# Performance work log

Measured on AMD Instinct MI355X. Metric: run time of the kernel, lower is better.

The kernel has to match this reference:

```python
import jax, jax.numpy as jnp
import numpy as np

NUM_EMBEDDINGS = 8192
EMBEDDING_DIM = 256
COMMITMENT_COST = 0.25
DECAY = 0.99
EPSILON = 1e-05


def setup_inputs() -> dict:
    key = jax.random.key(0)
    k1, k2 = jax.random.split(key)
    inputs = jax.random.normal(k1, (16384, EMBEDDING_DIM), dtype=jnp.float32)
    embedding = jax.random.normal(k2, (NUM_EMBEDDINGS, EMBEDDING_DIM), dtype=jnp.float32)
    ema_cluster_size = jnp.zeros((NUM_EMBEDDINGS,), dtype=jnp.float32)
    ema_w = embedding  # buffer initialized as a clone of the codebook
    return {"inputs": inputs, "embedding": embedding,
            "ema_cluster_size": ema_cluster_size, "ema_w": ema_w}


def reference(inputs, embedding, ema_cluster_size, ema_w):
    N, D = inputs.shape
    K = embedding.shape[0]

    x2 = jnp.sum(inputs * inputs, axis=1, keepdims=True)          # [N,1]
    e2 = jnp.sum(embedding * embedding, axis=1)                   # [K]
    d2 = x2 + e2[None, :] - 2.0 * (inputs @ embedding.T)          # [N,K]
    idx = jnp.argmin(d2, axis=1)                                  # [N]

    quantized_raw = embedding[idx]                                # [N,D]
    encodings = jax.nn.one_hot(idx, K, dtype=jnp.float32)         # [N,K]

    # cluster statistics (scatter-add instead of dense one-hot matmul)
    counts = jax.ops.segment_sum(jnp.ones((N,), jnp.float32), idx, num_segments=K)  # [K]
    dw = jax.ops.segment_sum(inputs, idx, num_segments=K)                            # [K,D]

    # EMA codebook update (training branch)
    ecs = ema_cluster_size * DECAY + (1.0 - DECAY) * counts
    n = jnp.sum(ecs)
    ecs = (ecs + EPSILON) / (n + K * EPSILON) * n
    new_ema_w = ema_w * DECAY + (1.0 - DECAY) * dw
    new_embedding = new_ema_w / ecs[:, None]

    # commitment loss (quantized detached)
    e_latent_loss = jnp.mean((jax.lax.stop_gradient(quantized_raw) - inputs) ** 2)
    loss = COMMITMENT_COST * e_latent_loss

    # straight-through estimator
    quantized = inputs + jax.lax.stop_gradient(quantized_raw - inputs)

    avg_probs = counts / N
    perplexity = jnp.exp(-jnp.sum(avg_probs * jnp.log(avg_probs + 1e-10)))

    return (loss, quantized, perplexity, encodings, new_embedding, ecs, new_ema_w)
```

## Files before the change

kernel.cpp:

```cpp
#include <hip/hip_runtime.h>
#include <cstdint>
#include <cstddef>

#define NROWS 16384
#define DDIM  256
#define KCODES 8192
#define MARGIN 1.5f

typedef short bf16x8 __attribute__((ext_vector_type(8)));
typedef float f32x4 __attribute__((ext_vector_type(4)));
typedef float f32x2 __attribute__((ext_vector_type(2)));

__device__ inline unsigned short f2bf(float f) {
  unsigned int u = __float_as_uint(f);
  return (unsigned short)((u + 0x7fffu + ((u >> 16) & 1u)) >> 16);
}

__device__ inline void ins2(float v, int i, float& v1, int& i1, float& v2, int& i2) {
  bool b1 = (v < v1) || (v == v1 && i < i1);
  bool b2 = (v < v2) || (v == v2 && i < i2);
  if (b1) { v2 = v1; i2 = i1; v1 = v; i1 = i; }
  else if (b2) { v2 = v; i2 = i; }
}

__global__ void k_prep(const float* __restrict__ inp, const float* __restrict__ emb,
                       unsigned short* __restrict__ Xb, unsigned short* __restrict__ Ebt,
                       float* __restrict__ x2, float* __restrict__ e2) {
  int wave = threadIdx.x >> 6, lane = threadIdx.x & 63;
  int row = blockIdx.x * 4 + wave;
  bool isx = row < NROWS;
  const float* src = isx ? (inp + (size_t)row * DDIM) : (emb + (size_t)(row - NROWS) * DDIM);
  float4 v = ((const float4*)src)[lane];
  ushort4 u; u.x = f2bf(v.x); u.y = f2bf(v.y); u.z = f2bf(v.z); u.w = f2bf(v.w);
  if (isx) {
    *(ushort4*)&Xb[(size_t)row * DDIM + lane * 4] = u;
  } else {
    int c = row - NROWS, ct = c >> 4, lc = c & 15;
    size_t off = (size_t)ct * 4096 + (lane >> 3) * 512 + lc * 32 + (lane & 7) * 4;
    *(ushort4*)&Ebt[off] = u;
  }
  float s = v.x * v.x + v.y * v.y + v.z * v.z + v.w * v.w;
#pragma unroll
  for (int o = 32; o >= 1; o >>= 1) s += __shfl_down(s, o, 64);
  if (lane == 0) { if (isx) x2[row] = s; else e2[row - NROWS] = s; }
}

#define DECL_SLOT(s) \
  float v1_##s = 3.4e38f, v2_##s = 3.4e38f; \
  int i1_##s = 0x7fffffff, i2_##s = 0x7fffffff;

#define UPD(s, a) { \
  float d = fmaf(-2.0f, (a), e2c); \
  if (d < v1_##s) { v2_##s = v1_##s; i2_##s = i1_##s; v1_##s = d; i1_##s = col; } \
  else if (d < v2_##s) { v2_##s = d; i2_##s = col; } }

#define RED_SLOT(s, mi, r) { \
  float a1 = v1_##s, a2 = v2_##s; int b1 = i1_##s, b2 = i2_##s; \
  for (int off = 1; off < 16; off <<= 1) { \
    float o1 = __shfl_xor(a1, off, 64); int p1 = __shfl_xor(b1, off, 64); \
    float o2 = __shfl_xor(a2, off, 64); int p2 = __shfl_xor(b2, off, 64); \
    ins2(o1, p1, a1, b1, a2, b2); ins2(o2, p2, a1, b1, a2, b2); } \
  if (lcol == 0) { \
    int row = row0 + (mi) * 16 + quad * 4 + (r); \
    size_t o = ((size_t)row * 8 + slice) * 2; \
    candv[o] = a1; candv[o + 1] = a2; candi[o] = b1; candi[o + 1] = b2; } }

__global__ __launch_bounds__(256, 2) void k_dist(
    const unsigned short* __restrict__ Xb, const unsigned short* __restrict__ Ebt,
    const float* __restrict__ e2,
    float* __restrict__ candv, int* __restrict__ candi) {
  const int lane = threadIdx.x & 63;
  const int w = threadIdx.x >> 6;
  const int lcol = lane & 15, quad = lane >> 4;
  const int row0 = (blockIdx.x >> 3) * 128 + w * 32;
  const int slice = blockIdx.x & 7;

  const unsigned short* ApA = Xb + (size_t)(row0 + lcol) * DDIM + quad * 8;
  const unsigned short* ApB = ApA + 16 * DDIM;
#define DECL_A(q) \
  bf16x8 A0_##q = *(const bf16x8*)(ApA + (q) * 32); \
  bf16x8 A1_##q = *(const bf16x8*)(ApB + (q) * 32);
  DECL_A(0) DECL_A(1) DECL_A(2) DECL_A(3) DECL_A(4) DECL_A(5) DECL_A(6) DECL_A(7)

  DECL_SLOT(0) DECL_SLOT(1) DECL_SLOT(2) DECL_SLOT(3)
  DECL_SLOT(4) DECL_SLOT(5) DECL_SLOT(6) DECL_SLOT(7)

  const unsigned short* Bbase = Ebt + (size_t)slice * 64 * 4096 + lcol * 32 + quad * 8;
  const float* e2p = e2 + slice * 1024 + lcol;
  const int colbase = slice * 1024 + lcol;

#pragma unroll 2
  for (int t = 0; t < 64; ++t) {
    const unsigned short* Bt = Bbase + (size_t)t * 4096;
    bf16x8 B0 = *(const bf16x8*)(Bt);
    bf16x8 B1 = *(const bf16x8*)(Bt + 512);
    bf16x8 B2 = *(const bf16x8*)(Bt + 1024);
    bf16x8 B3 = *(const bf16x8*)(Bt + 1536);
    bf16x8 B4 = *(const bf16x8*)(Bt + 2048);
    bf16x8 B5 = *(const bf16x8*)(Bt + 2560);
    bf16x8 B6 = *(const bf16x8*)(Bt + 3072);
    bf16x8 B7 = *(const bf16x8*)(Bt + 3584);
    float e2c = e2p[t * 16];
    f32x4 acc0 = {0.f, 0.f, 0.f, 0.f};
    f32x4 acc1 = {0.f, 0.f, 0.f, 0.f};
#define MM(q) \
    acc0 = __builtin_amdgcn_mfma_f32_16x16x32_bf16(A0_##q, B##q, acc0, 0, 0, 0); \
    acc1 = __builtin_amdgcn_mfma_f32_16x16x32_bf16(A1_##q, B##q, acc1, 0, 0, 0);
    MM(0) MM(1) MM(2) MM(3) MM(4) MM(5) MM(6) MM(7)
#undef MM
    const int col = colbase + t * 16;
    UPD(0, acc0[0]) UPD(1, acc0[1]) UPD(2, acc0[2]) UPD(3, acc0[3])
    UPD(4, acc1[0]) UPD(5, acc1[1]) UPD(6, acc1[2]) UPD(7, acc1[3])
  }

  RED_SLOT(0, 0, 0) RED_SLOT(1, 0, 1) RED_SLOT(2, 0, 2) RED_SLOT(3, 0, 3)
  RED_SLOT(4, 1, 0) RED_SLOT(5, 1, 1) RED_SLOT(6, 1, 2) RED_SLOT(7, 1, 3)
}

__global__ void k_selscat(const float* __restrict__ inp, const float* __restrict__ emb,
                          const float* __restrict__ x2, const float* __restrict__ e2,
                          const float* __restrict__ candv, const int* __restrict__ candi,
                          int* __restrict__ idxb,
                          float* __restrict__ out_quant,
                          float* __restrict__ counts, float* __restrict__ dw,
                          float* __restrict__ loss_acc) {
  __shared__ float wsum[4];
  int w = threadIdx.x >> 6, lane = threadIdx.x & 63;
  int row = blockIdx.x * 4 + w;
  float cv = 3.4e38f;
  int ci = 0x7fffffff;
  if (lane < 16) { cv = candv[(size_t)row * 16 + lane]; ci = candi[(size_t)row * 16 + lane]; }
  float m = cv;
#pragma unroll
  for (int o = 32; o >= 1; o >>= 1) m = fminf(m, __shfl_xor(m, o, 64));
  float thr = m + MARGIN;
  unsigned long long b = __ballot(cv <= thr);
  float4 x = *(const float4*)(inp + (size_t)row * DDIM + lane * 4);
  float x2r = x2[row];
  float bestv = 3.4e38f;
  int besti = 0x7fffffff;
  while (b) {
    int src = __ffsll(b) - 1; b &= b - 1;
    int j = __shfl(ci, src, 64);
    float4 e4 = *(const float4*)(emb + (size_t)j * DDIM + lane * 4);
    float p = x.x * e4.x + x.y * e4.y + x.z * e4.z + x.w * e4.w;
#pragma unroll
    for (int o = 32; o >= 1; o >>= 1) p += __shfl_xor(p, o, 64);
    float d2 = (x2r + e2[j]) - 2.0f * p;
    if (d2 < bestv || (d2 == bestv && j < besti)) { bestv = d2; besti = j; }
  }
  const int j = besti;
  if (lane == 0) idxb[row] = j;

  float4 e = *(const float4*)(emb + (size_t)j * DDIM + lane * 4);
  size_t qo = (size_t)row * DDIM + lane * 4;
  __builtin_nontemporal_store(x.x + (e.x - x.x), out_quant + qo + 0);
  __builtin_nontemporal_store(x.y + (e.y - x.y), out_quant + qo + 1);
  __builtin_nontemporal_store(x.z + (e.z - x.z), out_quant + qo + 2);
  __builtin_nontemporal_store(x.w + (e.w - x.w), out_quant + qo + 3);
  size_t dwo = (size_t)j * DDIM + lane * 4;
  atomicAdd(&dw[dwo + 0], x.x);
  atomicAdd(&dw[dwo + 1], x.y);
  atomicAdd(&dw[dwo + 2], x.z);
  atomicAdd(&dw[dwo + 3], x.w);
  float d0 = e.x - x.x, d1 = e.y - x.y, d2 = e.z - x.z, d3 = e.w - x.w;
  float s = d0 * d0 + d1 * d1 + d2 * d2 + d3 * d3;
#pragma unroll
  for (int o = 32; o >= 1; o >>= 1) s += __shfl_down(s, o, 64);
  if (lane == 0) {
    atomicAdd(&counts[j], 1.0f);
    wsum[w] = s;
  }
  __syncthreads();
  if (threadIdx.x == 0) atomicAdd(loss_acc, wsum[0] + wsum[1] + wsum[2] + wsum[3]);
}

__global__ __launch_bounds__(256) void k_enc(const int* __restrict__ idxb,
                                             float* __restrict__ out_enc) {
  const int row = blockIdx.x;
  const int tid = threadIdx.x;
  const int j = idxb[row];
  float* base = out_enc + (size_t)row * KCODES;
#pragma unroll
  for (int i = 0; i < 8; ++i) {
    int q = i * 256 + tid;
    if (q < 2047) {
      int f0 = 2 + q * 4;
      f32x4 v;
      v[0] = (j == f0 + 0) ? 1.0f : 0.0f;
      v[1] = (j == f0 + 1) ? 1.0f : 0.0f;
      v[2] = (j == f0 + 2) ? 1.0f : 0.0f;
      v[3] = (j == f0 + 3) ? 1.0f : 0.0f;
      __builtin_nontemporal_store(v, (f32x4*)(base + f0));
    }
  }
  if (tid == 0) {
    f32x2 head = {j == 0 ? 1.0f : 0.0f, j == 1 ? 1.0f : 0.0f};
    f32x2 tail = {j == 8190 ? 1.0f : 0.0f, j == 8191 ? 1.0f : 0.0f};
    __builtin_nontemporal_store(head, (f32x2*)base);
    __builtin_nontemporal_store(tail, (f32x2*)(base + 8190));
  }
}

__global__ void k_stats(const float* __restrict__ counts, const float* __restrict__ ema_cs,
                        const float* __restrict__ loss_acc,
                        float* __restrict__ out_loss, float* __restrict__ out_perp,
                        float* __restrict__ out_ecs) {
  __shared__ float red[8];
  int tid = threadIdx.x;
  float ln = 0.0f, lp = 0.0f;
  for (int k = tid; k < KCODES; k += 256) {
    float c = counts[k];
    float er = ema_cs[k] * 0.99f + 0.01f * c;
    ln += er;
    float p = c * (1.0f / 16384.0f);
    lp += p * logf(p + 1e-10f);
  }
  int lane = tid & 63, wave = tid >> 6;
#pragma unroll
  for (int o = 32; o >= 1; o >>= 1) {
    ln += __shfl_down(ln, o, 64);
    lp += __shfl_down(lp, o, 64);
  }
  if (lane == 0) { red[wave] = ln; red[wave + 4] = lp; }
  __syncthreads();
  float n = red[0] + red[1] + red[2] + red[3];
  float plsum = red[4] + red[5] + red[6] + red[7];
  float denom = n + 0.08192f;
  for (int k = tid; k < KCODES; k += 256) {
    float c = counts[k];
    float er = ema_cs[k] * 0.99f + 0.01f * c;
    out_ecs[k] = (er + 1e-5f) / denom * n;
  }
  if (tid == 0) {
    out_loss[0] = 0.25f * (loss_acc[0] / 4194304.0f);
    out_perp[0] = expf(-plsum);
  }
}

__global__ void k_update(const float* __restrict__ ema_w, const float* __restrict__ dw,
                         const float* __restrict__ ecs,
                         float* __restrict__ out_emaw, float* __restrict__ out_emb) {
  size_t i = ((size_t)blockIdx.x * blockDim.x + threadIdx.x) * 4;
  int k = (int)(i >> 8);
  float4 w = *(const float4*)(ema_w + i);
  float4 d = *(const float4*)(dw + i);
  float ec = ecs[k];
  float nw0 = w.x * 0.99f + 0.01f * d.x;
  float nw1 = w.y * 0.99f + 0.01f * d.y;
  float nw2 = w.z * 0.99f + 0.01f * d.z;
  float nw3 = w.w * 0.99f + 0.01f * d.w;
  f32x2 a0 = {nw0, nw1}, a1 = {nw2, nw3};
  f32x2 b0 = {nw0 / ec, nw1 / ec}, b1 = {nw2 / ec, nw3 / ec};
  __builtin_nontemporal_store(a0, (f32x2*)(out_emaw + i));
  __builtin_nontemporal_store(a1, (f32x2*)(out_emaw + i + 2));
  __builtin_nontemporal_store(b0, (f32x2*)(out_emb + i));
  __builtin_nontemporal_store(b1, (f32x2*)(out_emb + i + 2));
}

extern "C" void kernel_launch(void* const* d_in, const int* in_sizes, int n_in,
                              void* d_out, int out_size, void* d_ws, size_t ws_size,
                              hipStream_t stream) {
  const float* inp = (const float*)d_in[0];
  const float* emb = (const float*)d_in[1];
  const float* emacs = (const float*)d_in[2];
  const float* emaw = (const float*)d_in[3];

  float* out = (float*)d_out;
  float* out_loss = out;
  float* out_quant = out + 1;
  float* out_perp = out_quant + (size_t)NROWS * DDIM;
  float* out_enc = out_perp + 1;
  float* out_emb = out_enc + (size_t)NROWS * KCODES;
  float* out_ecs = out_emb + (size_t)KCODES * DDIM;
  float* out_emaw = out_ecs + KCODES;

  char* p = (char*)d_ws;
  unsigned short* Xb = (unsigned short*)p; p += (size_t)NROWS * DDIM * 2;
  unsigned short* Ebt = (unsigned short*)p; p += (size_t)KCODES * DDIM * 2;
  float* x2 = (float*)p; p += (size_t)NROWS * 4;
  float* e2 = (float*)p; p += (size_t)KCODES * 4;
  float* candv = (float*)p; p += (size_t)NROWS * 16 * 4;
  int* candi = (int*)p; p += (size_t)NROWS * 16 * 4;
  float* dw = (float*)p; p += (size_t)KCODES * DDIM * 4;
  float* counts = (float*)p; p += (size_t)KCODES * 4;
  float* loss_acc = (float*)p; p += 16;
  int* idxb = (int*)p; p += (size_t)NROWS * 4;

  (void)hipMemsetAsync(dw, 0, ((size_t)KCODES * DDIM + KCODES + 4) * sizeof(float), stream);

  k_prep<<<(NROWS + KCODES) / 4, 256, 0, stream>>>(inp, emb, Xb, Ebt, x2, e2);
  k_dist<<<1024, 256, 0, stream>>>(Xb, Ebt, e2, candv, candi);
  k_selscat<<<NROWS / 4, 256, 0, stream>>>(inp, emb, x2, e2, candv, candi, idxb,
                                           out_quant, counts, dw, loss_acc);
  k_enc<<<NROWS, 256, 0, stream>>>(idxb, out_enc);
  k_stats<<<1, 256, 0, stream>>>(counts, emacs, loss_acc, out_loss, out_perp, out_ecs);
  k_update<<<(KCODES * DDIM) / 1024, 256, 0, stream>>>(emaw, dw, out_ecs, out_emaw, out_emb);
}
```

Measured before the change: 972.6 us.

## Stage codebook tiles through double-buffered LDS with async global-to-LDS loads

Result: faster. 927.8 us (-4.6%).

```diff
diff --git a/kernel.cpp b/kernel.cpp
--- a/kernel.cpp
+++ b/kernel.cpp
@@ -14,6 +14,12 @@
 __device__ inline unsigned short f2bf(float f) {
   unsigned int u = __float_as_uint(f);
   return (unsigned short)((u + 0x7fffu + ((u >> 16) & 1u)) >> 16);
+}
+
+__device__ inline void gl_lds16(const void* g, void* l) {
+  __builtin_amdgcn_global_load_lds(
+      (const __attribute__((address_space(1))) unsigned int*)g,
+      (__attribute__((address_space(3))) unsigned int*)l, 16, 0, 0);
 }
 
 __device__ inline void ins2(float v, int i, float& v1, int& i1, float& v2, int& i2) {
@@ -69,11 +75,16 @@
     const unsigned short* __restrict__ Xb, const unsigned short* __restrict__ Ebt,
     const float* __restrict__ e2,
     float* __restrict__ candv, int* __restrict__ candi) {
-  const int lane = threadIdx.x & 63;
-  const int w = threadIdx.x >> 6;
+  __shared__ unsigned short Bs[2][4096];
+  __shared__ float se2[1024];
+  const int tid = threadIdx.x;
+  const int lane = tid & 63;
+  const int w = tid >> 6;
   const int lcol = lane & 15, quad = lane >> 4;
-  const int row0 = (blockIdx.x >> 3) * 128 + w * 32;
-  const int slice = blockIdx.x & 7;
+  const int rt = blockIdx.x >> 3, slice = blockIdx.x & 7;
+  const int row0 = rt * 128 + w * 32;
+
+  ((float4*)se2)[tid] = ((const float4*)(e2 + slice * 1024))[tid];
 
   const unsigned short* ApA = Xb + (size_t)(row0 + lcol) * DDIM + quad * 8;
   const unsigned short* ApB = ApA + 16 * DDIM;
@@ -85,22 +96,32 @@
   DECL_SLOT(0) DECL_SLOT(1) DECL_SLOT(2) DECL_SLOT(3)
   DECL_SLOT(4) DECL_SLOT(5) DECL_SLOT(6) DECL_SLOT(7)
 
-  const unsigned short* Bbase = Ebt + (size_t)slice * 64 * 4096 + lcol * 32 + quad * 8;
-  const float* e2p = e2 + slice * 1024 + lcol;
+  const unsigned short* Ebase = Ebt + (size_t)(slice * 64) * 4096;
+  const int inst0 = w * 2, inst1 = w * 2 + 1;
+
+  gl_lds16(Ebase + inst0 * 512 + lane * 8, &Bs[0][inst0 * 512]);
+  gl_lds16(Ebase + inst1 * 512 + lane * 8, &Bs[0][inst1 * 512]);
+
   const int colbase = slice * 1024 + lcol;
-
-#pragma unroll 2
+  int buf = 0;
   for (int t = 0; t < 64; ++t) {
-    const unsigned short* Bt = Bbase + (size_t)t * 4096;
-    bf16x8 B0 = *(const bf16x8*)(Bt);
-    bf16x8 B1 = *(const bf16x8*)(Bt + 512);
-    bf16x8 B2 = *(const bf16x8*)(Bt + 1024);
-    bf16x8 B3 = *(const bf16x8*)(Bt + 1536);
-    bf16x8 B4 = *(const bf16x8*)(Bt + 2048);
-    bf16x8 B5 = *(const bf16x8*)(Bt + 2560);
-    bf16x8 B6 = *(const bf16x8*)(Bt + 3072);
-    bf16x8 B7 = *(const bf16x8*)(Bt + 3584);
-    float e2c = e2p[t * 16];
+    __syncthreads();
+    if (t < 63) {
+      const unsigned short* Eg = Ebase + (size_t)(t + 1) * 4096;
+      gl_lds16(Eg + inst0 * 512 + lane * 8, &Bs[buf ^ 1][inst0 * 512]);
+      gl_lds16(Eg + inst1 * 512 + lane * 8, &Bs[buf ^ 1][inst1 * 512]);
+    }
+    const unsigned short* Bt = &Bs[buf][0];
+    const int laneoff = lcol * 32 + quad * 8;
+    bf16x8 B0 = *(const bf16x8*)(Bt + laneoff);
+    bf16x8 B1 = *(const bf16x8*)(Bt + 512 + laneoff);
+    bf16x8 B2 = *(const bf16x8*)(Bt + 1024 + laneoff);
+    bf16x8 B3 = *(const bf16x8*)(Bt + 1536 + laneoff);
+    bf16x8 B4 = *(const bf16x8*)(Bt + 2048 + laneoff);
+    bf16x8 B5 = *(const bf16x8*)(Bt + 2560 + laneoff);
+    bf16x8 B6 = *(const bf16x8*)(Bt + 3072 + laneoff);
+    bf16x8 B7 = *(const bf16x8*)(Bt + 3584 + laneoff);
+    float e2c = se2[t * 16 + lcol];
     f32x4 acc0 = {0.f, 0.f, 0.f, 0.f};
     f32x4 acc1 = {0.f, 0.f, 0.f, 0.f};
 #define MM(q) \
@@ -111,6 +132,7 @@
     const int col = colbase + t * 16;
     UPD(0, acc0[0]) UPD(1, acc0[1]) UPD(2, acc0[2]) UPD(3, acc0[3])
     UPD(4, acc1[0]) UPD(5, acc1[1]) UPD(6, acc1[2]) UPD(7, acc1[3])
+    buf ^= 1;
   }
 
   RED_SLOT(0, 0, 0) RED_SLOT(1, 0, 1) RED_SLOT(2, 0, 2) RED_SLOT(3, 0, 3)
```
